# Kernel optimization log

Measured on AMD Instinct MI355X. Metric: run time of the kernel, lower is better.

Reference implementation:

```python
import jax, jax.numpy as jnp
import numpy as np

B, C, N = 8, 256, 4096

def setup_inputs() -> dict:
    key = jax.random.key(0)
    k1, k2, k3 = jax.random.split(key, 3)
    pts_feat = jax.random.normal(k1, (B, C, N), dtype=jnp.float32)
    # Conv1d(channels, channels, 1, bias=False) weight is [C_out, C_in, 1] -> store as [C_out, C_in]
    scale = 1.0 / np.sqrt(C)
    Wq = jax.random.uniform(k2, (C, C), dtype=jnp.float32, minval=-scale, maxval=scale)
    Wk = jax.random.uniform(k3, (C, C), dtype=jnp.float32, minval=-scale, maxval=scale)
    return {"pts_feat": pts_feat, "Wq": Wq, "Wk": Wk}

def reference(pts_feat, Wq, Wk):
    # 1x1 conv == channel-wise matmul. x_q: [B, N, C], x_k: [B, C, N]
    x_q = jnp.einsum('bcn,dc->bnd', pts_feat, Wq)
    x_k = jnp.einsum('bcn,dc->bdn', pts_feat, Wk)
    logits = jnp.einsum('bnc,bcm->bnm', x_q, x_k)          # [B, N, N]
    attn = jax.nn.softmax(logits, axis=-1)
    attn = attn / (1e-8 + attn.sum(axis=-1, keepdims=True))
    # torch.einsum('bnn,bnc->bnc', attn, feat) takes the DIAGONAL of attn
    # and scales each point's raw feature vector by it (no contraction).
    diag = jnp.diagonal(attn, axis1=1, axis2=2)            # [B, N]
    x_attn = pts_feat * diag[:, None, :]                   # [B, C, N]
    return x_attn
```

## Files before the change

### kernel.cpp

```cpp
#include <hip/hip_runtime.h>
#include <hip/hip_bf16.h>
#include <cstdint>

#define B_ 8
#define C_ 256
#define N_ 4096

typedef __bf16 bf16;
typedef __bf16 bf16x8 __attribute__((ext_vector_type(8)));
typedef float f32x4 __attribute__((ext_vector_type(4)));
typedef float f32x16 __attribute__((ext_vector_type(16)));
typedef unsigned int u32;

__device__ __forceinline__ void async_ld16(const void* g, void* l) {
  __builtin_amdgcn_global_load_lds(
      (const __attribute__((address_space(1))) void*)g,
      (__attribute__((address_space(3))) void*)l, 16, 0, 0);
}

__device__ __forceinline__ float bh2f(unsigned short u) {
  union { u32 i; float f; } x; x.i = ((u32)u) << 16; return x.f;
}
__device__ __forceinline__ unsigned short f2bh(float f) {
  union { float f; u32 i; } x; x.f = f;
  u32 i = x.i + 0x7fffu + ((x.i >> 16) & 1u);
  return (unsigned short)(i >> 16);
}

__device__ __forceinline__ bool wave_sniff_fp32(const unsigned short* p) {
  int l = threadIdx.x & 63;
  unsigned short u = p[2 * l];
  int e = (u >> 7) & 0xff;
  unsigned long long m = __ballot(e >= 112 && e <= 142);
  return __popcll(m) < 32;
}

__global__ __launch_bounds__(256) void k_pre(const void* __restrict__ Wqv,
                                             const void* __restrict__ Wkv,
                                             const void* __restrict__ Fv,
                                             unsigned short* __restrict__ Mt,
                                             unsigned short* __restrict__ Ft) {
  __shared__ float wkcol[C_];
  __shared__ unsigned short tile[64 * 66];
  int bid = blockIdx.x;
  int t = threadIdx.x;
  if (bid < 256) {
    bool fq = wave_sniff_fp32((const unsigned short*)Wqv);
    bool fk = wave_sniff_fp32((const unsigned short*)Wkv);
    int d = bid, c = t;
    if (fk)
      wkcol[c] = ((const float*)Wkv)[c * C_ + d];
    else
      wkcol[c] = bh2f(((const unsigned short*)Wkv)[c * C_ + d]);
    __syncthreads();
    float acc = 0.f;
    if (fq) {
      for (int e0 = 0; e0 < C_; e0 += 16) {
        float wq[16];
#pragma unroll
        for (int j = 0; j < 16; ++j) wq[j] = ((const float*)Wqv)[(e0 + j) * C_ + c];
#pragma unroll
        for (int j = 0; j < 16; ++j) acc += wkcol[e0 + j] * wq[j];
      }
    } else {
      for (int e0 = 0; e0 < C_; e0 += 16) {
        float wq[16];
#pragma unroll
        for (int j = 0; j < 16; ++j) wq[j] = bh2f(((const unsigned short*)Wqv)[(e0 + j) * C_ + c]);
#pragma unroll
        for (int j = 0; j < 16; ++j) acc += wkcol[e0 + j] * wq[j];
      }
    }
    Mt[(size_t)d * C_ + c] = f2bh(acc);
    return;
  }
  bool f32 = wave_sniff_fp32((const unsigned short*)Fv);
  int id = bid - 256;
  int n0 = (id & 63) * 64, c0 = ((id >> 6) & 3) * 64, b = id >> 8;
#pragma unroll
  for (int p = 0; p < 2; ++p) {
    int c = (t >> 3) + 32 * p;
    int n = (t & 7) * 8;
    size_t off = (size_t)(b * C_ + c0 + c) * N_ + n0 + n;
    unsigned short vals[8];
    if (f32) {
      const float* src = (const float*)Fv + off;
      float4 v0 = *(const float4*)(src);
      float4 v1 = *(const float4*)(src + 4);
      vals[0] = f2bh(v0.x); vals[1] = f2bh(v0.y); vals[2] = f2bh(v0.z); vals[3] = f2bh(v0.w);
      vals[4] = f2bh(v1.x); vals[5] = f2bh(v1.y); vals[6] = f2bh(v1.z); vals[7] = f2bh(v1.w);
    } else {
      uint4 v = *(const uint4*)((const unsigned short*)Fv + off);
      vals[0] = (unsigned short)(v.x & 0xffffu); vals[1] = (unsigned short)(v.x >> 16);
      vals[2] = (unsigned short)(v.y & 0xffffu); vals[3] = (unsigned short)(v.y >> 16);
      vals[4] = (unsigned short)(v.z & 0xffffu); vals[5] = (unsigned short)(v.z >> 16);
      vals[6] = (unsigned short)(v.w & 0xffffu); vals[7] = (unsigned short)(v.w >> 16);
    }
#pragma unroll
    for (int s = 0; s < 8; ++s) tile[c * 66 + n + s] = vals[s];
  }
  __syncthreads();
#pragma unroll
  for (int p = 0; p < 4; ++p) {
    int n = (t >> 4) + 16 * p;
    int cq = (t & 15) * 4;
    unsigned short e0 = tile[(cq + 0) * 66 + n];
    unsigned short e1 = tile[(cq + 1) * 66 + n];
    unsigned short e2 = tile[(cq + 2) * 66 + n];
    unsigned short e3 = tile[(cq + 3) * 66 + n];
    uint2 o;
    o.x = ((u32)e1 << 16) | e0;
    o.y = ((u32)e3 << 16) | e2;
    *(uint2*)(Ft + ((size_t)(b * N_ + n0 + n) * C_ + c0 + cq)) = o;
  }
}

__global__ __launch_bounds__(256, 2) void k_proj(const bf16* __restrict__ Ft,
                                                 const bf16* __restrict__ Mt,
                                                 bf16* __restrict__ G) {
  __shared__ bf16 As[8 * 128 * 32];
  int n0 = blockIdx.x * 128;
  int b = blockIdx.y;
  int d0 = blockIdx.z * 128;
  int t = threadIdx.x, w = t >> 6, l = t & 63;
  int lr = l & 15, lq = l >> 4;
  int wn = w * 32;
  const size_t fbase = (size_t)b * N_ * C_;

  int schunk = ((t & 3) ^ ((t >> 3) & 3)) * 8;
#pragma unroll
  for (int kc = 0; kc < 8; ++kc)
#pragma unroll
    for (int r = 0; r < 2; ++r)
      async_ld16(Ft + fbase + (size_t)(n0 + r * 64 + (t >> 2)) * C_ + kc * 32 + schunk,
                 As + kc * 4096 + (r * 256 + t) * 8);

  bf16x8 bb[2][8];
#pragma unroll
  for (int j = 0; j < 2; ++j)
#pragma unroll
    for (int kc = 0; kc < 8; ++kc)
      bb[j][kc] = *(const bf16x8*)(Mt + (size_t)(d0 + wn + 16 * j + lr) * C_ + kc * 32 + lq * 8);

  __syncthreads();
  int rchunk = (lq ^ ((lr >> 1) & 3)) * 8;
  f32x4 acc[8][2] = {};
#pragma unroll
  for (int kc = 0; kc < 8; ++kc) {
#pragma unroll
    for (int i = 0; i < 8; ++i) {
      bf16x8 a = *(const bf16x8*)(As + kc * 4096 + (16 * i + lr) * 32 + rchunk);
#pragma unroll
      for (int j = 0; j < 2; ++j)
        acc[i][j] = __builtin_amdgcn_mfma_f32_16x16x32_bf16(a, bb[j][kc], acc[i][j], 0, 0, 0);
    }
  }
#pragma unroll
  for (int i = 0; i < 8; ++i)
#pragma unroll
    for (int j = 0; j < 2; ++j)
#pragma unroll
      for (int r = 0; r < 4; ++r) {
        int row = n0 + 16 * i + lq * 4 + r;
        int col = d0 + wn + 16 * j + lr;
        G[fbase + (size_t)row * C_ + col] = (bf16)acc[i][j][r];
      }
}

__global__ __launch_bounds__(256, 4) void k_attn(const bf16* __restrict__ G,
                                                 const bf16* __restrict__ Ft,
                                                 float* __restrict__ snn,
                                                 float* __restrict__ lsum) {
  __shared__ bf16 Ks[32 * 256];
  int bid = blockIdx.x;
  int b = bid & 7, q = (bid >> 3) & 7, ntile = bid >> 6;
  int n0 = ntile * 128;
  int t = threadIdx.x, w = t >> 6, l = t & 63;
  int lm = l & 31, hi = l >> 5;
  int wrow = w * 32;
  const size_t gbase = (size_t)b * N_ * C_;

  bf16x8 a[16];
#pragma unroll
  for (int kc = 0; kc < 16; ++kc)
    a[kc] = *(const bf16x8*)(G + gbase + (size_t)(n0 + wrow + lm) * C_ + kc * 16 + hi * 8);

  float part[16];
#pragma unroll
  for (int s = 0; s < 16; ++s) part[s] = 0.f;

  int m_base = q * 512;

  for (int it = 0; it < 16; ++it) {
    int m0 = m_base + it * 32;
    __syncthreads();
#pragma unroll
    for (int u = 0; u < 4; ++u) {
      int s = w * 4 + u;
      int row = 2 * s + hi;
      int c = (lm ^ (row & 7)) * 8;
      async_ld16(Ft + gbase + (size_t)(m0 + row) * C_ + c, Ks + s * 512);
    }
    __syncthreads();
    f32x16 acc = {};
#pragma unroll
    for (int kc = 0; kc < 16; ++kc) {
      int gp = (kc * 2 + hi) ^ (lm & 7);
      bf16x8 bb = *(const bf16x8*)(Ks + lm * 256 + gp * 8);
      acc = __builtin_amdgcn_mfma_f32_32x32x16_bf16(a[kc], bb, acc, 0, 0, 0);
    }
    bool dit = (m0 == n0 + wrow);
#pragma unroll
    for (int reg = 0; reg < 16; ++reg) {
      float e = __expf(acc[reg]);
      part[reg] += e;
      if (dit) {
        int rloc = (reg & 3) + 8 * (reg >> 2) + 4 * hi;
        if (lm == rloc) snn[b * N_ + n0 + wrow + rloc] = e;
      }
    }
  }

#pragma unroll
  for (int s = 0; s < 16; ++s) {
    float v = part[s];
    v += __shfl_xor(v, 1);
    v += __shfl_xor(v, 2);
    v += __shfl_xor(v, 4);
    v += __shfl_xor(v, 8);
    v += __shfl_xor(v, 16);
    part[s] = v;
  }
  if (lm == 0) {
#pragma unroll
    for (int reg = 0; reg < 16; ++reg) {
      int rloc = (reg & 3) + 8 * (reg >> 2) + 4 * hi;
      lsum[((size_t)q * B_ + b) * N_ + n0 + wrow + rloc] = part[reg];
    }
  }
}

__global__ __launch_bounds__(256) void k_scale(const void* __restrict__ Fv,
                                               const float* __restrict__ snn,
                                               const float* __restrict__ lsum,
                                               void* __restrict__ Outv) {
  bool f32 = wave_sniff_fp32((const unsigned short*)Fv);
  int g = blockIdx.x * 256 + threadIdx.x;
  size_t base = (size_t)g * 8;
  int n = (int)(base & (N_ - 1));
  int b = (int)(base >> 20);
  float4 s0 = *(const float4*)(snn + (size_t)b * N_ + n);
  float4 s1 = *(const float4*)(snn + (size_t)b * N_ + n + 4);
  float ls[8];
#pragma unroll
  for (int k = 0; k < 8; ++k) ls[k] = 0.f;
#pragma unroll
  for (int p = 0; p < 8; ++p) {
    float4 l0 = *(const float4*)(lsum + ((size_t)p * B_ + b) * N_ + n);
    float4 l1 = *(const float4*)(lsum + ((size_t)p * B_ + b) * N_ + n + 4);
    ls[0] += l0.x; ls[1] += l0.y; ls[2] += l0.z; ls[3] += l0.w;
    ls[4] += l1.x; ls[5] += l1.y; ls[6] += l1.z; ls[7] += l1.w;
  }
  const float c1 = 1.0f + 1e-8f;
  float dd[8];
  dd[0] = s0.x / (ls[0] * c1); dd[1] = s0.y / (ls[1] * c1);
  dd[2] = s0.z / (ls[2] * c1); dd[3] = s0.w / (ls[3] * c1);
  dd[4] = s1.x / (ls[4] * c1); dd[5] = s1.y / (ls[5] * c1);
  dd[6] = s1.z / (ls[6] * c1); dd[7] = s1.w / (ls[7] * c1);
  if (f32) {
    const float* F = (const float*)Fv + base;
    float* O = (float*)Outv + base;
    float4 a0 = *(const float4*)(F);
    float4 a1 = *(const float4*)(F + 4);
    float4 o0, o1;
    o0.x = a0.x * dd[0]; o0.y = a0.y * dd[1]; o0.z = a0.z * dd[2]; o0.w = a0.w * dd[3];
    o1.x = a1.x * dd[4]; o1.y = a1.y * dd[5]; o1.z = a1.z * dd[6]; o1.w = a1.w * dd[7];
    *(float4*)(O) = o0;
    *(float4*)(O + 4) = o1;
  } else {
    uint4 v = *(const uint4*)((const unsigned short*)Fv + base);
    u32 vv[4] = {v.x, v.y, v.z, v.w};
    u32 o[4];
#pragma unroll
    for (int k = 0; k < 4; ++k) {
      float lo = bh2f((unsigned short)(vv[k] & 0xffffu)) * dd[2 * k];
      float hi = bh2f((unsigned short)(vv[k] >> 16)) * dd[2 * k + 1];
      o[k] = ((u32)f2bh(hi) << 16) | f2bh(lo);
    }
    uint4 ov; ov.x = o[0]; ov.y = o[1]; ov.z = o[2]; ov.w = o[3];
    *(uint4*)((unsigned short*)Outv + base) = ov;
  }
}

extern "C" void kernel_launch(void* const* d_in, const int* in_sizes, int n_in,
                              void* d_out, int out_size, void* d_ws, size_t ws_size,
                              hipStream_t stream) {
  (void)in_sizes; (void)n_in; (void)out_size; (void)ws_size;
  const void* F = d_in[0];
  const void* Wq = d_in[1];
  const void* Wk = d_in[2];
  char* ws = (char*)d_ws;
  bf16* Ft = (bf16*)(ws);
  bf16* G = (bf16*)(ws + (16u << 20));
  char* tail = ws + (32u << 20);
  float* snn = (float*)(tail);
  float* lsum = (float*)(tail + 131072);
  bf16* Mt = (bf16*)(tail + 131072 + 1048576);

  k_pre<<<256 + 2048, 256, 0, stream>>>(Wq, Wk, F, (unsigned short*)Mt, (unsigned short*)Ft);
  k_proj<<<dim3(N_ / 128, B_, 2), 256, 0, stream>>>(Ft, Mt, G);
  k_attn<<<2048, 256, 0, stream>>>(G, Ft, snn, lsum);
  k_scale<<<(B_ * C_ * N_ / 8) / 256, 256, 0, stream>>>(F, snn, lsum, d_out);
}
```

Before: 202.5 us.

## Widen attention key tile to 64 columns and halve projection row tile

The attention kernel now stages 64 key rows per iteration and issues two 32x32 MFMAs per A fragment. It splits the key dimension into 4 partitions instead of 8, which halves the grid and the partial-sum buffer that k_scale reduces. The projection kernel uses 64-row tiles with more blocks and higher occupancy. The aim is to amortize barriers and A-fragment reuse over more keys and cut partial-sum traffic, at the cost of more LDS and fewer blocks for the attention kernel.

```diff
diff --git a/kernel.cpp b/kernel.cpp
--- a/kernel.cpp
+++ b/kernel.cpp
@@ -115,11 +115,11 @@
   }
 }
 
-__global__ __launch_bounds__(256, 2) void k_proj(const bf16* __restrict__ Ft,
+__global__ __launch_bounds__(256, 4) void k_proj(const bf16* __restrict__ Ft,
                                                  const bf16* __restrict__ Mt,
                                                  bf16* __restrict__ G) {
-  __shared__ bf16 As[8 * 128 * 32];
-  int n0 = blockIdx.x * 128;
+  __shared__ bf16 As[8 * 64 * 32];
+  int n0 = blockIdx.x * 64;
   int b = blockIdx.y;
   int d0 = blockIdx.z * 128;
   int t = threadIdx.x, w = t >> 6, l = t & 63;
@@ -127,13 +127,12 @@
   int wn = w * 32;
   const size_t fbase = (size_t)b * N_ * C_;
 
+  int srow = t >> 2;
   int schunk = ((t & 3) ^ ((t >> 3) & 3)) * 8;
 #pragma unroll
   for (int kc = 0; kc < 8; ++kc)
-#pragma unroll
-    for (int r = 0; r < 2; ++r)
-      async_ld16(Ft + fbase + (size_t)(n0 + r * 64 + (t >> 2)) * C_ + kc * 32 + schunk,
-                 As + kc * 4096 + (r * 256 + t) * 8);
+    async_ld16(Ft + fbase + (size_t)(n0 + srow) * C_ + kc * 32 + schunk,
+               As + kc * 2048 + t * 8);
 
   bf16x8 bb[2][8];
 #pragma unroll
@@ -144,19 +143,19 @@
 
   __syncthreads();
   int rchunk = (lq ^ ((lr >> 1) & 3)) * 8;
-  f32x4 acc[8][2] = {};
+  f32x4 acc[4][2] = {};
 #pragma unroll
   for (int kc = 0; kc < 8; ++kc) {
 #pragma unroll
-    for (int i = 0; i < 8; ++i) {
-      bf16x8 a = *(const bf16x8*)(As + kc * 4096 + (16 * i + lr) * 32 + rchunk);
+    for (int i = 0; i < 4; ++i) {
+      bf16x8 a = *(const bf16x8*)(As + kc * 2048 + (16 * i + lr) * 32 + rchunk);
 #pragma unroll
       for (int j = 0; j < 2; ++j)
         acc[i][j] = __builtin_amdgcn_mfma_f32_16x16x32_bf16(a, bb[j][kc], acc[i][j], 0, 0, 0);
     }
   }
 #pragma unroll
-  for (int i = 0; i < 8; ++i)
+  for (int i = 0; i < 4; ++i)
 #pragma unroll
     for (int j = 0; j < 2; ++j)
 #pragma unroll
@@ -171,9 +170,9 @@
                                                  const bf16* __restrict__ Ft,
                                                  float* __restrict__ snn,
                                                  float* __restrict__ lsum) {
-  __shared__ bf16 Ks[32 * 256];
+  __shared__ bf16 Ks[64 * 256];
   int bid = blockIdx.x;
-  int b = bid & 7, q = (bid >> 3) & 7, ntile = bid >> 6;
+  int b = bid & 7, q = (bid >> 3) & 3, ntile = bid >> 5;
   int n0 = ntile * 128;
   int t = threadIdx.x, w = t >> 6, l = t & 63;
   int lm = l & 31, hi = l >> 5;
@@ -189,34 +188,40 @@
 #pragma unroll
   for (int s = 0; s < 16; ++s) part[s] = 0.f;
 
-  int m_base = q * 512;
+  int m_base = q * 1024;
 
   for (int it = 0; it < 16; ++it) {
-    int m0 = m_base + it * 32;
+    int m0 = m_base + it * 64;
     __syncthreads();
 #pragma unroll
-    for (int u = 0; u < 4; ++u) {
-      int s = w * 4 + u;
-      int row = 2 * s + hi;
-      int c = (lm ^ (row & 7)) * 8;
-      async_ld16(Ft + gbase + (size_t)(m0 + row) * C_ + c, Ks + s * 512);
+    for (int i = 0; i < 8; ++i) {
+      int row = i * 8 + (t >> 5);
+      int gsrc = (t & 31) ^ (row & 31);
+      async_ld16(Ft + gbase + (size_t)(m0 + row) * C_ + gsrc * 8,
+                 Ks + i * 2048 + t * 8);
     }
     __syncthreads();
-    f32x16 acc = {};
+    f32x16 acc[2] = {};
 #pragma unroll
     for (int kc = 0; kc < 16; ++kc) {
-      int gp = (kc * 2 + hi) ^ (lm & 7);
-      bf16x8 bb = *(const bf16x8*)(Ks + lm * 256 + gp * 8);
-      acc = __builtin_amdgcn_mfma_f32_32x32x16_bf16(a[kc], bb, acc, 0, 0, 0);
-    }
-    bool dit = (m0 == n0 + wrow);
-#pragma unroll
-    for (int reg = 0; reg < 16; ++reg) {
-      float e = __expf(acc[reg]);
-      part[reg] += e;
-      if (dit) {
-        int rloc = (reg & 3) + 8 * (reg >> 2) + 4 * hi;
-        if (lm == rloc) snn[b * N_ + n0 + wrow + rloc] = e;
+      int gp = (kc * 2 + hi) ^ lm;
+#pragma unroll
+      for (int mt = 0; mt < 2; ++mt) {
+        bf16x8 bb = *(const bf16x8*)(Ks + (mt * 32 + lm) * 256 + gp * 8);
+        acc[mt] = __builtin_amdgcn_mfma_f32_32x32x16_bf16(a[kc], bb, acc[mt], 0, 0, 0);
+      }
+    }
+#pragma unroll
+    for (int mt = 0; mt < 2; ++mt) {
+      bool dit = (m0 + mt * 32 == n0 + wrow);
+#pragma unroll
+      for (int reg = 0; reg < 16; ++reg) {
+        float e = __expf(acc[mt][reg]);
+        part[reg] += e;
+        if (dit) {
+          int rloc = (reg & 3) + 8 * (reg >> 2) + 4 * hi;
+          if (lm == rloc) snn[b * N_ + n0 + wrow + rloc] = e;
+        }
       }
     }
   }
@@ -255,7 +260,7 @@
 #pragma unroll
   for (int k = 0; k < 8; ++k) ls[k] = 0.f;
 #pragma unroll
-  for (int p = 0; p < 8; ++p) {
+  for (int p = 0; p < 4; ++p) {
     float4 l0 = *(const float4*)(lsum + ((size_t)p * B_ + b) * N_ + n);
     float4 l1 = *(const float4*)(lsum + ((size_t)p * B_ + b) * N_ + n + 4);
     ls[0] += l0.x; ls[1] += l0.y; ls[2] += l0.z; ls[3] += l0.w;
@@ -305,10 +310,10 @@
   char* tail = ws + (32u << 20);
   float* snn = (float*)(tail);
   float* lsum = (float*)(tail + 131072);
-  bf16* Mt = (bf16*)(tail + 131072 + 1048576);
+  bf16* Mt = (bf16*)(tail + 131072 + 524288);
 
   k_pre<<<256 + 2048, 256, 0, stream>>>(Wq, Wk, F, (unsigned short*)Mt, (unsigned short*)Ft);
-  k_proj<<<dim3(N_ / 128, B_, 2), 256, 0, stream>>>(Ft, Mt, G);
-  k_attn<<<2048, 256, 0, stream>>>(G, Ft, snn, lsum);
+  k_proj<<<dim3(N_ / 64, B_, 2), 256, 0, stream>>>(Ft, Mt, G);
+  k_attn<<<1024, 256, 0, stream>>>(G, Ft, snn, lsum);
   k_scale<<<(B_ * C_ * N_ / 8) / 256, 256, 0, stream>>>(F, snn, lsum, d_out);
 }
```

After: 218.0 us. 7.6% more time.
